# Kernel tuning notes

Measured on AMD Instinct MI355X. Metric: run time of the kernel, lower is better.

The kernel has to match this reference:

```python
import jax, jax.numpy as jnp
import numpy as np

N_NODES = 100000
N_EDGES = 1600000
DIM = 128
N_LAYERS = 3


def setup_inputs() -> dict:
    key = jax.random.key(0)
    ks = jax.random.split(key, 8)
    h0 = jax.random.normal(ks[0], (N_NODES, 117), dtype=jnp.float32)
    src = jax.random.randint(ks[1], (N_EDGES,), 0, N_NODES, dtype=jnp.int32)
    dst = jax.random.randint(ks[2], (N_EDGES,), 0, N_NODES, dtype=jnp.int32)
    s_in = 1.0 / np.sqrt(117.0)
    s_h = 1.0 / np.sqrt(float(DIM))
    W_in = jax.random.uniform(ks[3], (117, DIM), jnp.float32, -s_in, s_in)
    b_in = jax.random.uniform(ks[4], (DIM,), jnp.float32, -s_in, s_in)
    W_self = jax.random.uniform(ks[5], (N_LAYERS, DIM, DIM), jnp.float32, -s_h, s_h)
    W_neigh = jax.random.uniform(ks[6], (N_LAYERS, DIM, DIM), jnp.float32, -s_h, s_h)
    b_sage = jax.random.uniform(ks[7], (N_LAYERS, DIM), jnp.float32, -s_h, s_h)
    return {"h0": h0, "src": src, "dst": dst, "W_in": W_in, "b_in": b_in,
            "W_self": W_self, "W_neigh": W_neigh, "b_sage": b_sage}


def _sage_mean(x, src, dst, Wse, Wne, b):
    # GraphSAGE with mean aggregator: h = x @ W_self + mean_neigh(x) @ W_neigh + b
    neigh_sum = jax.ops.segment_sum(x[src], dst, num_segments=N_NODES)  # [N, D]
    deg = jax.ops.segment_sum(jnp.ones((src.shape[0],), x.dtype), dst,
                              num_segments=N_NODES)  # [N]
    neigh_mean = neigh_sum / jnp.maximum(deg, 1.0)[:, None]
    return x @ Wse + neigh_mean @ Wne + b


def reference(h0, src, dst, W_in, b_in, W_self, W_neigh, b_sage):
    # f_in: Linear(117,128) + Tanh, per node
    h = jnp.tanh(h0 @ W_in + b_in)  # [N, 128]
    # config = [128,'relu'] x 3 -> SAGEConv then relu, three times
    for l in range(N_LAYERS):
        h = _sage_mean(h, src, dst, W_self[l], W_neigh[l], b_sage[l])
        h = jax.nn.relu(h)
    return h
```

## Files before the change

### kernel.cpp

```cpp
#include <hip/hip_runtime.h>
#include <hip/hip_bf16.h>
#include <cstdint>
#include <cstddef>

#define NN 100000
#define NE 1600000
#define DIM 128
#define KIN 117
#define NLAYERS 3
#define NB 98


__global__ void k_hist(const int* __restrict__ dst, int* __restrict__ cnt) {
  int i = blockIdx.x * blockDim.x + threadIdx.x;
  if (i < NE) atomicAdd(&cnt[dst[i]], 1);
}

__global__ void k_scanA(const int* __restrict__ cnt, int* __restrict__ part,
                        int* __restrict__ bsum) {
  __shared__ int sh[1024];
  int tid = threadIdx.x;
  int i = blockIdx.x * 1024 + tid;
  int v = (i < NN) ? cnt[i] : 0;
  sh[tid] = v;
  __syncthreads();
  for (int off = 1; off < 1024; off <<= 1) {
    int t = (tid >= off) ? sh[tid - off] : 0;
    __syncthreads();
    sh[tid] += t;
    __syncthreads();
  }
  if (i < NN) part[i] = sh[tid] - v;
  if (tid == 1023) bsum[blockIdx.x] = sh[1023];
}

__global__ void k_scanB(const int* __restrict__ bsum, int* __restrict__ boff,
                        int* __restrict__ rptr) {
  if (threadIdx.x == 0 && blockIdx.x == 0) {
    int run = 0;
    for (int b = 0; b < NB; ++b) { boff[b] = run; run += bsum[b]; }
    rptr[NN] = run;
  }
}

__global__ void k_scanC(const int* __restrict__ part, const int* __restrict__ boff,
                        int* __restrict__ rptr, int* __restrict__ cursor) {
  int i = blockIdx.x * 1024 + threadIdx.x;
  if (i < NN) {
    int v = part[i] + boff[i >> 10];
    rptr[i] = v;
    cursor[i] = v;
  }
}

__global__ void k_scatter(const int* __restrict__ src, const int* __restrict__ dst,
                          int* __restrict__ cursor, int* __restrict__ ssrc) {
  int i = blockIdx.x * blockDim.x + threadIdx.x;
  if (i < NE) {
    int p = atomicAdd(&cursor[dst[i]], 1);
    ssrc[p] = src[i];
  }
}


__global__ __launch_bounds__(256) void k_agg(const float* __restrict__ x,
                                             const int* __restrict__ rptr,
                                             const int* __restrict__ ssrc,
                                             float* __restrict__ mean) {
  int gid = blockIdx.x * blockDim.x + threadIdx.x;
  int node = __builtin_amdgcn_readfirstlane(gid >> 6);
  int lane = threadIdx.x & 63;
  if (node >= NN) return;
  int beg = __builtin_amdgcn_readfirstlane(rptr[node]);
  int end = __builtin_amdgcn_readfirstlane(rptr[node + 1]);
  int c0 = lane * 2;
  float ax = 0.f, ay = 0.f;
  int e = beg;
  for (; e + 3 < end; e += 4) {
    int s0 = __builtin_amdgcn_readfirstlane(ssrc[e]);
    int s1 = __builtin_amdgcn_readfirstlane(ssrc[e + 1]);
    int s2 = __builtin_amdgcn_readfirstlane(ssrc[e + 2]);
    int s3 = __builtin_amdgcn_readfirstlane(ssrc[e + 3]);
    float2 v0 = *reinterpret_cast<const float2*>(x + (size_t)s0 * DIM + c0);
    float2 v1 = *reinterpret_cast<const float2*>(x + (size_t)s1 * DIM + c0);
    float2 v2 = *reinterpret_cast<const float2*>(x + (size_t)s2 * DIM + c0);
    float2 v3 = *reinterpret_cast<const float2*>(x + (size_t)s3 * DIM + c0);
    ax += (v0.x + v1.x) + (v2.x + v3.x);
    ay += (v0.y + v1.y) + (v2.y + v3.y);
  }
  for (; e < end; ++e) {
    int s0 = __builtin_amdgcn_readfirstlane(ssrc[e]);
    float2 v0 = *reinterpret_cast<const float2*>(x + (size_t)s0 * DIM + c0);
    ax += v0.x;
    ay += v0.y;
  }
  int deg = end - beg;
  float inv = 1.0f / (float)(deg > 0 ? deg : 1);
  *reinterpret_cast<float2*>(mean + (size_t)node * DIM + c0) =
      make_float2(ax * inv, ay * inv);
}


template <int ACT, bool TWO>
__global__ __launch_bounds__(256) void k_gemm(
    const float* __restrict__ A, int lda, int K,
    const float* __restrict__ W,
    const float* __restrict__ A2,
    const float* __restrict__ W2,
    const float* __restrict__ bias,
    float* __restrict__ out, int M) {
  __shared__ float Xs[32][130];
  __shared__ float Ws[32][140];
  const int tid = threadIdx.x;
  const int trow = tid >> 4;
  const int tcol = tid & 15;
  const int m0 = blockIdx.x * 128;

  float acc[8][8];
#pragma unroll
  for (int i = 0; i < 8; ++i)
#pragma unroll
    for (int j = 0; j < 8; ++j) acc[i][j] = 0.f;

  const int npass = TWO ? 2 : 1;
  for (int pass = 0; pass < npass; ++pass) {
    const float* Ap = pass ? A2 : A;
    const float* Wp = pass ? W2 : W;
    const int ld = pass ? DIM : lda;
    const int Kp = pass ? DIM : K;
    for (int kt = 0; kt < Kp; kt += 32) {
      {
        int r = tid >> 1;
        int h = tid & 1;
        int row = m0 + r;
        int kbase = kt + h * 16;
        const float* srcp = Ap + (size_t)row * ld + kbase;
        if (row < M && (ld & 3) == 0 && kbase + 15 < Kp) {
#pragma unroll
          for (int j4 = 0; j4 < 4; ++j4) {
            float4 v = *reinterpret_cast<const float4*>(srcp + j4 * 4);
            Xs[h * 16 + j4 * 4 + 0][r] = v.x;
            Xs[h * 16 + j4 * 4 + 1][r] = v.y;
            Xs[h * 16 + j4 * 4 + 2][r] = v.z;
            Xs[h * 16 + j4 * 4 + 3][r] = v.w;
          }
        } else {
#pragma unroll
          for (int j = 0; j < 16; ++j) {
            int k = kbase + j;
            float v = 0.f;
            if (row < M && k < Kp) v = srcp[j];
            Xs[h * 16 + j][r] = v;
          }
        }
      }
      {
        int kk = tid >> 3;
        int seg = tid & 7;
        int k = kt + kk;
        if (k < Kp) {
          const float* wsrc = Wp + (size_t)k * DIM + seg * 16;
#pragma unroll
          for (int j4 = 0; j4 < 4; ++j4) {
            float4 v = *reinterpret_cast<const float4*>(wsrc + j4 * 4);
            *reinterpret_cast<float4*>(&Ws[kk][seg * 16 + j4 * 4]) = v;
          }
        } else {
#pragma unroll
          for (int j = 0; j < 16; ++j) Ws[kk][seg * 16 + j] = 0.f;
        }
      }
      __syncthreads();
#pragma unroll
      for (int k = 0; k < 32; ++k) {
        float2 t0 = *reinterpret_cast<const float2*>(&Xs[k][trow * 8 + 0]);
        float2 t1 = *reinterpret_cast<const float2*>(&Xs[k][trow * 8 + 2]);
        float2 t2 = *reinterpret_cast<const float2*>(&Xs[k][trow * 8 + 4]);
        float2 t3 = *reinterpret_cast<const float2*>(&Xs[k][trow * 8 + 6]);
        float4 b0 = *reinterpret_cast<const float4*>(&Ws[k][tcol * 4]);
        float4 b1 = *reinterpret_cast<const float4*>(&Ws[k][64 + tcol * 4]);
        float a[8] = {t0.x, t0.y, t1.x, t1.y, t2.x, t2.y, t3.x, t3.y};
        float b[8] = {b0.x, b0.y, b0.z, b0.w, b1.x, b1.y, b1.z, b1.w};
#pragma unroll
        for (int i = 0; i < 8; ++i)
#pragma unroll
          for (int j = 0; j < 8; ++j) acc[i][j] = fmaf(a[i], b[j], acc[i][j]);
      }
      __syncthreads();
    }
  }

  float4 bb0 = *reinterpret_cast<const float4*>(bias + tcol * 4);
  float4 bb1 = *reinterpret_cast<const float4*>(bias + 64 + tcol * 4);
  float bv[8] = {bb0.x, bb0.y, bb0.z, bb0.w, bb1.x, bb1.y, bb1.z, bb1.w};
#pragma unroll
  for (int i = 0; i < 8; ++i) {
    int row = m0 + trow * 8 + i;
    if (row < M) {
      float v[8];
#pragma unroll
      for (int j = 0; j < 8; ++j) {
        float t = acc[i][j] + bv[j];
        if (ACT == 0) {
          t = tanhf(t);
        } else {
          t = fmaxf(t, 0.f);
        }
        v[j] = t;
      }
      *reinterpret_cast<float4*>(out + (size_t)row * DIM + tcol * 4) =
          make_float4(v[0], v[1], v[2], v[3]);
      *reinterpret_cast<float4*>(out + (size_t)row * DIM + 64 + tcol * 4) =
          make_float4(v[4], v[5], v[6], v[7]);
    }
  }
}


extern "C" void kernel_launch(void* const* d_in, const int* in_sizes, int n_in,
                              void* d_out, int out_size, void* d_ws, size_t ws_size,
                              hipStream_t stream) {
  const float* h0 = (const float*)d_in[0];
  const int* srcp = (const int*)d_in[1];
  const int* dstp = (const int*)d_in[2];
  const float* W_in = (const float*)d_in[3];
  const float* b_in = (const float*)d_in[4];
  const float* W_self = (const float*)d_in[5];
  const float* W_neigh = (const float*)d_in[6];
  const float* b_sage = (const float*)d_in[7];
  float* outf = (float*)d_out;

  char* p = (char*)d_ws;
  auto alloc = [&](size_t bytes) {
    char* r = p;
    p += (bytes + 255) & ~(size_t)255;
    return r;
  };
  float* mean = (float*)alloc((size_t)NN * DIM * 4);
  float* hA = (float*)alloc((size_t)NN * DIM * 4);
  int* cnt = (int*)alloc((size_t)NN * 4);
  int* part = (int*)alloc((size_t)NN * 4);
  int* rptr = (int*)alloc((size_t)(NN + 1) * 4);
  int* cursor = (int*)alloc((size_t)NN * 4);
  int* ssrcS = (int*)alloc((size_t)NE * 4);
  int* bsum = (int*)alloc((size_t)NB * 4);
  int* boff = (int*)alloc((size_t)NB * 4);

  hipMemsetAsync(cnt, 0, (size_t)NN * 4, stream);
  k_hist<<<(NE + 255) / 256, 256, 0, stream>>>(dstp, cnt);
  k_scanA<<<NB, 1024, 0, stream>>>(cnt, part, bsum);
  k_scanB<<<1, 64, 0, stream>>>(bsum, boff, rptr);
  k_scanC<<<NB, 1024, 0, stream>>>(part, boff, rptr, cursor);
  k_scatter<<<(NE + 255) / 256, 256, 0, stream>>>(srcp, dstp, cursor, ssrcS);

  const int GB = (NN + 127) / 128;

  k_gemm<0, false><<<GB, 256, 0, stream>>>(h0, KIN, KIN, W_in, nullptr, nullptr,
                                           b_in, hA, NN);

  for (int l = 0; l < NLAYERS; ++l) {
    const float* x = (l == 1) ? outf : hA;
    float* o = (l == 1) ? hA : outf;
    const float* Wse = W_self + (size_t)l * DIM * DIM;
    const float* Wne = W_neigh + (size_t)l * DIM * DIM;
    const float* bs = b_sage + (size_t)l * DIM;
    k_agg<<<(NN * 64 + 255) / 256, 256, 0, stream>>>(x, rptr, ssrcS, mean);
    k_gemm<1, true><<<GB, 256, 0, stream>>>(x, DIM, DIM, Wse, mean, Wne, bs, o, NN);
  }
}
```

Measured before the change: 1.023 ms.

## Replace FP32 SIMT GEMM with split-bf16 MFMA GEMM and prepacked weights

Moves the per-layer dense GEMMs from scalar FMA loops onto bf16 MFMA instructions. FP32 accuracy is approximated by splitting each operand into high and low bf16 parts and summing three products. A new prep kernel packs all weight matrices into bf16 hi/lo fragment layout once per call. Activations are split on the fly when staged into shared memory. The risk is small precision loss and output stores that are now scalar and less coalesced.

```diff
diff --git a/kernel.cpp b/kernel.cpp
--- a/kernel.cpp
+++ b/kernel.cpp
@@ -9,6 +9,20 @@
 #define KIN 117
 #define NLAYERS 3
 #define NB 98
+#define NMAT 7
+
+typedef __attribute__((ext_vector_type(8))) short s16x8;
+typedef __attribute__((ext_vector_type(8))) __bf16 bf16x8;
+typedef __attribute__((ext_vector_type(4))) float f32x4;
+
+__device__ __forceinline__ unsigned short f2bf(float f) {
+  unsigned int u = __float_as_uint(f);
+  unsigned int r = (u + 0x7fffu + ((u >> 16) & 1u)) >> 16;
+  return (unsigned short)r;
+}
+__device__ __forceinline__ float bf2f(unsigned short b) {
+  return __uint_as_float(((unsigned int)b) << 16);
+}
 
 
 __global__ void k_hist(const int* __restrict__ dst, int* __restrict__ cnt) {
@@ -101,117 +115,154 @@
 }
 
 
+__global__ void k_wprep(const float* __restrict__ W_in,
+                        const float* __restrict__ W_self,
+                        const float* __restrict__ W_neigh,
+                        unsigned short* __restrict__ Wfrag) {
+  int bid = blockIdx.x;
+  int mat = bid >> 7;
+  int k = bid & 127;
+  int col = threadIdx.x;
+  float v = 0.f;
+  if (mat == 0) {
+    if (k < KIN) v = W_in[(size_t)k * DIM + col];
+  } else if (mat <= 3) {
+    v = W_self[(size_t)(mat - 1) * DIM * DIM + (size_t)k * DIM + col];
+  } else {
+    v = W_neigh[(size_t)(mat - 4) * DIM * DIM + (size_t)k * DIM + col];
+  }
+  unsigned short hb = f2bf(v);
+  unsigned short lb = f2bf(v - bf2f(hb));
+  int kt = k >> 5, k8 = (k >> 3) & 3, j = k & 7;
+  size_t base = ((size_t)(mat * 4 + kt) * 2) * 4096 + ((size_t)k8 * 128 + col) * 8 + j;
+  Wfrag[base] = hb;
+  Wfrag[base + 4096] = lb;
+}
+
+
 template <int ACT, bool TWO>
-__global__ __launch_bounds__(256) void k_gemm(
-    const float* __restrict__ A, int lda, int K,
-    const float* __restrict__ W,
+__global__ __launch_bounds__(256) void k_gemm_mfma(
+    const float* __restrict__ A, int lda, int Kvalid,
+    const unsigned short* __restrict__ Wf0,
     const float* __restrict__ A2,
-    const float* __restrict__ W2,
+    const unsigned short* __restrict__ Wf1,
     const float* __restrict__ bias,
     float* __restrict__ out, int M) {
-  __shared__ float Xs[32][130];
-  __shared__ float Ws[32][140];
+  __shared__ s16x8 Ah[512], Al[512], Bh[512], Bl[512];
   const int tid = threadIdx.x;
-  const int trow = tid >> 4;
-  const int tcol = tid & 15;
+  const int lane = tid & 63;
+  const int w = tid >> 6;
+  const int wr = (w >> 1) * 64, wc = (w & 1) * 64;
+  const int l15 = lane & 15, l4 = lane >> 4;
   const int m0 = blockIdx.x * 128;
 
-  float acc[8][8];
-#pragma unroll
-  for (int i = 0; i < 8; ++i)
-#pragma unroll
-    for (int j = 0; j < 8; ++j) acc[i][j] = 0.f;
-
-  const int npass = TWO ? 2 : 1;
-  for (int pass = 0; pass < npass; ++pass) {
+  f32x4 acc[4][4];
+#pragma unroll
+  for (int r = 0; r < 4; ++r)
+#pragma unroll
+    for (int c = 0; c < 4; ++c) acc[r][c] = (f32x4){0.f, 0.f, 0.f, 0.f};
+
+  const int srow = tid >> 1;
+  const int shalf = tid & 1;
+
+  for (int pass = 0; pass < (TWO ? 2 : 1); ++pass) {
     const float* Ap = pass ? A2 : A;
-    const float* Wp = pass ? W2 : W;
+    const unsigned short* Wp = pass ? Wf1 : Wf0;
     const int ld = pass ? DIM : lda;
-    const int Kp = pass ? DIM : K;
-    for (int kt = 0; kt < Kp; kt += 32) {
+    const int Kv = pass ? DIM : Kvalid;
+    for (int kt = 0; kt < 4; ++kt) {
+      __syncthreads();
       {
-        int r = tid >> 1;
-        int h = tid & 1;
-        int row = m0 + r;
-        int kbase = kt + h * 16;
-        const float* srcp = Ap + (size_t)row * ld + kbase;
-        if (row < M && (ld & 3) == 0 && kbase + 15 < Kp) {
-#pragma unroll
-          for (int j4 = 0; j4 < 4; ++j4) {
-            float4 v = *reinterpret_cast<const float4*>(srcp + j4 * 4);
-            Xs[h * 16 + j4 * 4 + 0][r] = v.x;
-            Xs[h * 16 + j4 * 4 + 1][r] = v.y;
-            Xs[h * 16 + j4 * 4 + 2][r] = v.z;
-            Xs[h * 16 + j4 * 4 + 3][r] = v.w;
+        int kbase = kt * 32 + shalf * 16;
+        float xv[16];
+        const int row = m0 + srow;
+        if (row < M && (ld & 3) == 0 && kbase + 16 <= Kv) {
+          const float* sp = Ap + (size_t)row * ld + kbase;
+#pragma unroll
+          for (int q = 0; q < 4; ++q) {
+            float4 v = *reinterpret_cast<const float4*>(sp + q * 4);
+            xv[q * 4 + 0] = v.x; xv[q * 4 + 1] = v.y;
+            xv[q * 4 + 2] = v.z; xv[q * 4 + 3] = v.w;
           }
         } else {
 #pragma unroll
-          for (int j = 0; j < 16; ++j) {
-            int k = kbase + j;
-            float v = 0.f;
-            if (row < M && k < Kp) v = srcp[j];
-            Xs[h * 16 + j][r] = v;
+          for (int i = 0; i < 16; ++i) {
+            int k = kbase + i;
+            xv[i] = (row < M && k < Kv) ? Ap[(size_t)row * ld + k] : 0.f;
           }
         }
+#pragma unroll
+        for (int q = 0; q < 2; ++q) {
+          s16x8 hv, lv;
+#pragma unroll
+          for (int j = 0; j < 8; ++j) {
+            float xf = xv[q * 8 + j];
+            unsigned short hb = f2bf(xf);
+            unsigned short lb = f2bf(xf - bf2f(hb));
+            hv[j] = (short)hb;
+            lv[j] = (short)lb;
+          }
+          int slot = (2 * shalf + q) * 128 + srow;
+          Ah[slot] = hv;
+          Al[slot] = lv;
+        }
       }
       {
-        int kk = tid >> 3;
-        int seg = tid & 7;
-        int k = kt + kk;
-        if (k < Kp) {
-          const float* wsrc = Wp + (size_t)k * DIM + seg * 16;
-#pragma unroll
-          for (int j4 = 0; j4 < 4; ++j4) {
-            float4 v = *reinterpret_cast<const float4*>(wsrc + j4 * 4);
-            *reinterpret_cast<float4*>(&Ws[kk][seg * 16 + j4 * 4]) = v;
-          }
-        } else {
-#pragma unroll
-          for (int j = 0; j < 16; ++j) Ws[kk][seg * 16 + j] = 0.f;
+        const s16x8* gW = reinterpret_cast<const s16x8*>(Wp + (size_t)kt * 8192);
+#pragma unroll
+        for (int r = 0; r < 2; ++r) {
+          int s = r * 256 + tid;
+          Bh[s] = gW[s];
+          Bl[s] = gW[512 + s];
         }
       }
       __syncthreads();
-#pragma unroll
-      for (int k = 0; k < 32; ++k) {
-        float2 t0 = *reinterpret_cast<const float2*>(&Xs[k][trow * 8 + 0]);
-        float2 t1 = *reinterpret_cast<const float2*>(&Xs[k][trow * 8 + 2]);
-        float2 t2 = *reinterpret_cast<const float2*>(&Xs[k][trow * 8 + 4]);
-        float2 t3 = *reinterpret_cast<const float2*>(&Xs[k][trow * 8 + 6]);
-        float4 b0 = *reinterpret_cast<const float4*>(&Ws[k][tcol * 4]);
-        float4 b1 = *reinterpret_cast<const float4*>(&Ws[k][64 + tcol * 4]);
-        float a[8] = {t0.x, t0.y, t1.x, t1.y, t2.x, t2.y, t3.x, t3.y};
-        float b[8] = {b0.x, b0.y, b0.z, b0.w, b1.x, b1.y, b1.z, b1.w};
-#pragma unroll
-        for (int i = 0; i < 8; ++i)
-#pragma unroll
-          for (int j = 0; j < 8; ++j) acc[i][j] = fmaf(a[i], b[j], acc[i][j]);
-      }
-      __syncthreads();
+      s16x8 ah[4], al_[4], bh[4], bl[4];
+#pragma unroll
+      for (int r = 0; r < 4; ++r) {
+        int off = l4 * 128 + wr + r * 16 + l15;
+        ah[r] = Ah[off];
+        al_[r] = Al[off];
+      }
+#pragma unroll
+      for (int c = 0; c < 4; ++c) {
+        int off = l4 * 128 + wc + c * 16 + l15;
+        bh[c] = Bh[off];
+        bl[c] = Bl[off];
+      }
+#pragma unroll
+      for (int r = 0; r < 4; ++r)
+#pragma unroll
+        for (int c = 0; c < 4; ++c) {
+          acc[r][c] = __builtin_amdgcn_mfma_f32_16x16x32_bf16(
+              __builtin_bit_cast(bf16x8, ah[r]), __builtin_bit_cast(bf16x8, bh[c]),
+              acc[r][c], 0, 0, 0);
+          acc[r][c] = __builtin_amdgcn_mfma_f32_16x16x32_bf16(
+              __builtin_bit_cast(bf16x8, ah[r]), __builtin_bit_cast(bf16x8, bl[c]),
+              acc[r][c], 0, 0, 0);
+          acc[r][c] = __builtin_amdgcn_mfma_f32_16x16x32_bf16(
+              __builtin_bit_cast(bf16x8, al_[r]), __builtin_bit_cast(bf16x8, bh[c]),
+              acc[r][c], 0, 0, 0);
+        }
     }
   }
 
-  float4 bb0 = *reinterpret_cast<const float4*>(bias + tcol * 4);
-  float4 bb1 = *reinterpret_cast<const float4*>(bias + 64 + tcol * 4);
-  float bv[8] = {bb0.x, bb0.y, bb0.z, bb0.w, bb1.x, bb1.y, bb1.z, bb1.w};
-#pragma unroll
-  for (int i = 0; i < 8; ++i) {
-    int row = m0 + trow * 8 + i;
-    if (row < M) {
-      float v[8];
-#pragma unroll
-      for (int j = 0; j < 8; ++j) {
-        float t = acc[i][j] + bv[j];
-        if (ACT == 0) {
-          t = tanhf(t);
-        } else {
-          t = fmaxf(t, 0.f);
-        }
-        v[j] = t;
-      }
-      *reinterpret_cast<float4*>(out + (size_t)row * DIM + tcol * 4) =
-          make_float4(v[0], v[1], v[2], v[3]);
-      *reinterpret_cast<float4*>(out + (size_t)row * DIM + 64 + tcol * 4) =
-          make_float4(v[4], v[5], v[6], v[7]);
+#pragma unroll
+  for (int c = 0; c < 4; ++c) {
+    int col = wc + c * 16 + l15;
+    float bv = bias[col];
+#pragma unroll
+    for (int r = 0; r < 4; ++r) {
+#pragma unroll
+      for (int i = 0; i < 4; ++i) {
+        int row = m0 + wr + r * 16 + l4 * 4 + i;
+        if (row < M) {
+          float v = acc[r][c][i] + bv;
+          if (ACT == 0) v = tanhf(v);
+          else v = fmaxf(v, 0.f);
+          out[(size_t)row * DIM + col] = v;
+        }
+      }
     }
   }
 }
@@ -245,6 +296,9 @@
   int* ssrcS = (int*)alloc((size_t)NE * 4);
   int* bsum = (int*)alloc((size_t)NB * 4);
   int* boff = (int*)alloc((size_t)NB * 4);
+  unsigned short* Wfrag = (unsigned short*)alloc((size_t)NMAT * 4 * 2 * 4096 * 2);
+
+  k_wprep<<<NMAT * 128, 128, 0, stream>>>(W_in, W_self, W_neigh, Wfrag);
 
   hipMemsetAsync(cnt, 0, (size_t)NN * 4, stream);
   k_hist<<<(NE + 255) / 256, 256, 0, stream>>>(dstp, cnt);
@@ -254,17 +308,17 @@
   k_scatter<<<(NE + 255) / 256, 256, 0, stream>>>(srcp, dstp, cursor, ssrcS);
 
   const int GB = (NN + 127) / 128;
-
-  k_gemm<0, false><<<GB, 256, 0, stream>>>(h0, KIN, KIN, W_in, nullptr, nullptr,
-                                           b_in, hA, NN);
+  auto wmat = [&](int mat) { return Wfrag + (size_t)mat * 32768; };
+
+  k_gemm_mfma<0, false><<<GB, 256, 0, stream>>>(h0, KIN, KIN, wmat(0), nullptr,
+                                                nullptr, b_in, hA, NN);
 
   for (int l = 0; l < NLAYERS; ++l) {
     const float* x = (l == 1) ? outf : hA;
     float* o = (l == 1) ? hA : outf;
-    const float* Wse = W_self + (size_t)l * DIM * DIM;
-    const float* Wne = W_neigh + (size_t)l * DIM * DIM;
     const float* bs = b_sage + (size_t)l * DIM;
     k_agg<<<(NN * 64 + 255) / 256, 256, 0, stream>>>(x, rptr, ssrcS, mean);
-    k_gemm<1, true><<<GB, 256, 0, stream>>>(x, DIM, DIM, Wse, mean, Wne, bs, o, NN);
-  }
-}
+    k_gemm_mfma<1, true><<<GB, 256, 0, stream>>>(x, DIM, DIM, wmat(1 + l), mean,
+                                                 wmat(4 + l), bs, o, NN);
+  }
+}
```

After: 845.2 us. 1.21x faster.
